# Kernel optimization log

Measured on AMD Instinct MI355X. Metric: run time of the kernel, lower is better.

The kernel has to match this reference:

```python
import jax, jax.numpy as jnp
import numpy as np

B, N, S = 8, 4096, 1024
D1, D2 = 128, 256
IN_CH, OUT_CH = D1 + D2, 256
BN_EPS = 1e-5


def setup_inputs() -> dict:
    key = jax.random.key(0)
    ks = jax.random.split(key, 12)
    inp = {
        "xyz1": jax.random.normal(ks[0], (B, N, 3), jnp.float32),
        "xyz2": jax.random.normal(ks[1], (B, S, 3), jnp.float32),
        "points1": jax.random.normal(ks[2], (B, N, D1), jnp.float32),
        "points2": jax.random.normal(ks[3], (B, S, D2), jnp.float32),
        # fuse: Conv1d(in_ch->out_ch, k=1) + BN
        "W_fuse": jax.random.normal(ks[4], (OUT_CH, IN_CH), jnp.float32) * (1.0 / np.sqrt(IN_CH)),
        "b_fuse": jnp.zeros((OUT_CH,), jnp.float32),
        "g_fuse": jnp.ones((OUT_CH,), jnp.float32),
        "bt_fuse": jnp.zeros((OUT_CH,), jnp.float32),
        # res block net1: Conv1d(out_ch->out_ch) + BN (res_expansion=1.0)
        "W1": jax.random.normal(ks[5], (OUT_CH, OUT_CH), jnp.float32) * (1.0 / np.sqrt(OUT_CH)),
        "b1": jnp.zeros((OUT_CH,), jnp.float32),
        "g1": jnp.ones((OUT_CH,), jnp.float32),
        "bt1": jnp.zeros((OUT_CH,), jnp.float32),
        # res block net2: Conv1d(out_ch->out_ch) + BN
        "W2": jax.random.normal(ks[6], (OUT_CH, OUT_CH), jnp.float32) * (1.0 / np.sqrt(OUT_CH)),
        "b2": jnp.zeros((OUT_CH,), jnp.float32),
        "g2": jnp.ones((OUT_CH,), jnp.float32),
        "bt2": jnp.zeros((OUT_CH,), jnp.float32),
    }
    return inp


def _bn(x, g, b):
    # BatchNorm1d training-mode forward: stats over (batch, length), x: [B, C, L]
    m = jnp.mean(x, axis=(0, 2), keepdims=True)
    v = jnp.var(x, axis=(0, 2), keepdims=True)
    return (x - m) * jax.lax.rsqrt(v + BN_EPS) * g[None, :, None] + b[None, :, None]


def _conv1x1(x, W, b):
    # x: [B, C_in, L], W: [C_out, C_in] -> [B, C_out, L]
    return jnp.einsum("oc,bcl->bol", W, x) + b[None, :, None]


def _gelu(x):
    return jax.nn.gelu(x, approximate=False)  # torch nn.GELU default (erf)


def reference(xyz1, xyz2, points1, points2,
              W_fuse, b_fuse, g_fuse, bt_fuse,
              W1, b1, g1, bt1, W2, b2, g2, bt2):
    # squared pairwise distances [B, N, S] without B x N x S x 3 intermediate
    d = (jnp.sum(xyz1 * xyz1, -1)[:, :, None]
         - 2.0 * jnp.einsum("bnc,bsc->bns", xyz1, xyz2)
         + jnp.sum(xyz2 * xyz2, -1)[:, None, :])
    # 3 nearest coarse points per dense point (== sort ascending, take first 3)
    neg_d3, idx = jax.lax.top_k(-d, 3)            # [B, N, 3]
    d3 = -neg_d3
    recip = 1.0 / (d3 + 1e-8)
    w = recip / jnp.sum(recip, axis=2, keepdims=True)  # [B, N, 3]
    gathered = points2[jnp.arange(points2.shape[0])[:, None, None], idx]  # [B, N, 3, D2]
    interp = jnp.sum(gathered * w[..., None], axis=2)  # [B, N, D2]

    new_points = jnp.concatenate([points1, interp], axis=-1)  # [B, N, D1+D2]
    x = jnp.transpose(new_points, (0, 2, 1))                   # [B, C, N]

    # fuse: conv-bn-gelu
    x = _gelu(_bn(_conv1x1(x, W_fuse, b_fuse), g_fuse, bt_fuse))
    # residual block: gelu(bn(conv(gelu(bn(conv(x))))) + x)
    y = _gelu(_bn(_conv1x1(x, W1, b1), g1, bt1))
    y = _bn(_conv1x1(y, W2, b2), g2, bt2)
    x = _gelu(y + x)

    return jnp.transpose(x, (0, 2, 1))  # [B, N, out_ch]
```

## Files before the change

kernel.cpp:

```cpp
#include <hip/hip_runtime.h>
#include <hip/hip_bf16.h>

constexpr int Bb = 8, Nn = 4096, Ss = 1024;
constexpr int D1 = 128, D2 = 256, KIN = 384, OC = 256;
constexpr int L = Bb * Nn;
constexpr float BN_EPS = 1e-5f;

typedef __attribute__((ext_vector_type(4))) float floatx4;
typedef __attribute__((ext_vector_type(8))) __bf16 bf16x8;

#define DEV __device__ __forceinline__

DEV float bf2f(unsigned short u) {
    union { unsigned int i; float f; } v; v.i = ((unsigned int)u) << 16; return v.f;
}
DEV unsigned short f2bf(float f) {
    union { float f; unsigned int i; } v; v.f = f;
    unsigned int x = v.i;
    return (unsigned short)((x + 0x7FFFu + ((x >> 16) & 1u)) >> 16);
}
DEV float gelu_f(float x) {
    float u = x * (0.7978845608f + 0.0356774081f * x * x);
    float t = __expf(-2.0f * u);
    return x * __builtin_amdgcn_rcpf(1.0f + t);
}

__global__ void k_probe(const unsigned int* __restrict__ w, int* __restrict__ flag) {
    if (threadIdx.x == 0 && blockIdx.x == 0) {
        int sane = 0;
        for (int i = 0; i < 64; ++i) {
            unsigned int lo = w[i] & 0xFFFFu;
            int e = (int)((lo >> 7) & 0xFF);
            if (e >= 100 && e <= 144) ++sane;
        }
        *flag = (sane >= 48) ? 0 : 1;
    }
}

__global__ void k_zero(float* p) {
    int i = blockIdx.x * 256 + threadIdx.x;
    if (i < 6 * 256) p[i] = 0.0f;
}

__global__ void k_prep_w(const void* __restrict__ src, unsigned short* __restrict__ dst,
                         int n, const int* __restrict__ dflag) {
    int i = blockIdx.x * 256 + threadIdx.x;
    if (i >= n) return;
    if (*dflag) dst[i] = f2bf(((const float*)src)[i]);
    else        dst[i] = ((const unsigned short*)src)[i];
}

DEV void merge3(float& d0, float& d1, float& d2, int& i0, int& i1, int& i2,
                float e0, float e1, float e2, int j0, int j1, int j2, bool pref) {
    float a0 = d0, a1 = d1, a2 = d2; int x0 = i0, x1 = i1, x2 = i2;
    float b0 = e0, b1 = e1;          int y0 = j0, y1 = j1;
    bool t = pref ? (a0 <= b0) : (a0 < b0);
    d0 = t ? a0 : b0; i0 = t ? x0 : y0;
    a0 = t ? a1 : a0; x0 = t ? x1 : x0;
    a1 = t ? a2 : a1; x1 = t ? x2 : x1;
    b0 = t ? b0 : b1; y0 = t ? y0 : y1;
    b1 = t ? b1 : e2; y1 = t ? y1 : j2;
    t = pref ? (a0 <= b0) : (a0 < b0);
    d1 = t ? a0 : b0; i1 = t ? x0 : y0;
    a0 = t ? a1 : a0; x0 = t ? x1 : x0;
    b0 = t ? b0 : b1; y0 = t ? y0 : y1;
    t = pref ? (a0 <= b0) : (a0 < b0);
    d2 = t ? a0 : b0; i2 = t ? x0 : y0;
}

__global__ __launch_bounds__(256) void k_nn(const void* __restrict__ xyz1_,
                                            const void* __restrict__ xyz2_,
                                            const int* __restrict__ dflag,
                                            int* __restrict__ nn_idx, float* __restrict__ nn_w) {
    __shared__ alignas(16) float s4[Ss * 4 + 32];
    int tid = threadIdx.x;
    int b = (blockIdx.x * 32) >> 12;
    bool isf = (*dflag != 0);

    if (isf) {
        const float* p2 = (const float*)xyz2_ + (size_t)b * Ss * 3;
        for (int i = tid; i < Ss * 3; i += 256) {
            int s = i / 3, k = i - s * 3;
            s4[s * 4 + k + ((s >> 7) << 2)] = p2[i];
        }
    } else {
        const unsigned short* p2 = (const unsigned short*)xyz2_ + (size_t)b * Ss * 3;
        for (int i = tid; i < Ss * 3; i += 256) {
            int s = i / 3, k = i - s * 3;
            s4[s * 4 + k + ((s >> 7) << 2)] = bf2f(p2[i]);
        }
    }
    __syncthreads();
    for (int s = tid; s < Ss; s += 256) {
        int a = s * 4 + ((s >> 7) << 2);
        float x = s4[a], y = s4[a + 1], z = s4[a + 2];
        s4[a + 3] = x * x + y * y + z * z;
    }
    __syncthreads();

    int part = tid & 7;
    int bn = blockIdx.x * 32 + (tid >> 3);
    float x1, y1, z1;
    if (isf) {
        const float* p1 = (const float*)xyz1_ + (size_t)bn * 3;
        x1 = p1[0]; y1 = p1[1]; z1 = p1[2];
    } else {
        const unsigned short* p1 = (const unsigned short*)xyz1_ + (size_t)bn * 3;
        x1 = bf2f(p1[0]); y1 = bf2f(p1[1]); z1 = bf2f(p1[2]);
    }
    float n1 = x1 * x1 + y1 * y1 + z1 * z1;

    float d0 = 3.4e38f, d1 = 3.4e38f, d2 = 3.4e38f;
    int i0 = 0, i1 = 0, i2 = 0;
    const float* sp = &s4[part * 516];
#pragma unroll 4
    for (int j = 0; j < 128; ++j) {
        float4 q = *(const float4*)(sp + j * 4);
        float d = n1 + q.w - 2.0f * (x1 * q.x + y1 * q.y + z1 * q.z);
        int s = part * 128 + j;
        bool c2 = d < d2, c1 = d < d1, c0 = d < d0;
        d2 = c1 ? d1 : (c2 ? d : d2); i2 = c1 ? i1 : (c2 ? s : i2);
        d1 = c0 ? d0 : (c1 ? d : d1); i1 = c0 ? i0 : (c1 ? s : i1);
        d0 = c0 ? d  : d0;            i0 = c0 ? s  : i0;
    }
#pragma unroll
    for (int m = 1; m <= 4; m <<= 1) {
        float e0 = __shfl_xor(d0, m, 64), e1 = __shfl_xor(d1, m, 64), e2 = __shfl_xor(d2, m, 64);
        int   j0 = __shfl_xor(i0, m, 64), j1 = __shfl_xor(i1, m, 64), j2 = __shfl_xor(i2, m, 64);
        bool pref = (part < (part ^ m));
        merge3(d0, d1, d2, i0, i1, i2, e0, e1, e2, j0, j1, j2, pref);
    }
    if (part == 0) {
        float r0 = 1.0f / (d0 + 1e-8f), r1 = 1.0f / (d1 + 1e-8f), r2 = 1.0f / (d2 + 1e-8f);
        float rs = 1.0f / (r0 + r1 + r2);
        nn_idx[bn * 3 + 0] = i0; nn_idx[bn * 3 + 1] = i1; nn_idx[bn * 3 + 2] = i2;
        nn_w[bn * 3 + 0] = r0 * rs; nn_w[bn * 3 + 1] = r1 * rs; nn_w[bn * 3 + 2] = r2 * rs;
    }
}

__global__ __launch_bounds__(256) void k_build_x(const void* __restrict__ points1_,
                                                 const void* __restrict__ points2_,
                                                 const int* __restrict__ dflag,
                                                 const int* __restrict__ nn_idx,
                                                 const float* __restrict__ nn_w,
                                                 unsigned short* __restrict__ X) {
    int tid = threadIdx.x;
    int pt = blockIdx.x * 4 + (tid >> 6);
    int lane = tid & 63;
    int b = pt >> 12;
    bool isf = (*dflag != 0);

    int i0 = nn_idx[pt * 3], i1 = nn_idx[pt * 3 + 1], i2 = nn_idx[pt * 3 + 2];
    float w0 = nn_w[pt * 3], w1 = nn_w[pt * 3 + 1], w2 = nn_w[pt * 3 + 2];
    int c = lane * 4;

    if (isf) {
        const float* p1 = (const float*)points1_ + (size_t)pt * D1;
        float2 v = *(const float2*)(p1 + lane * 2);
        unsigned int packed = (unsigned int)f2bf(v.x) | ((unsigned int)f2bf(v.y) << 16);
        ((unsigned int*)(X + (size_t)pt * KIN))[lane] = packed;

        const float* base = (const float*)points2_;
        const float* r0 = base + ((size_t)(b * Ss + i0)) * D2 + c;
        const float* r1 = base + ((size_t)(b * Ss + i1)) * D2 + c;
        const float* r2 = base + ((size_t)(b * Ss + i2)) * D2 + c;
        float4 a0 = *(const float4*)r0;
        float4 a1 = *(const float4*)r1;
        float4 a2 = *(const float4*)r2;
        uint2 out;
        unsigned short* uo = (unsigned short*)&out;
        uo[0] = f2bf(w0 * a0.x + w1 * a1.x + w2 * a2.x);
        uo[1] = f2bf(w0 * a0.y + w1 * a1.y + w2 * a2.y);
        uo[2] = f2bf(w0 * a0.z + w1 * a1.z + w2 * a2.z);
        uo[3] = f2bf(w0 * a0.w + w1 * a1.w + w2 * a2.w);
        *(uint2*)(X + (size_t)pt * KIN + D1 + c) = out;
    } else {
        const unsigned short* p1 = (const unsigned short*)points1_;
        ((unsigned int*)(X + (size_t)pt * KIN))[lane] =
            ((const unsigned int*)(p1 + (size_t)pt * D1))[lane];

        const unsigned short* base = (const unsigned short*)points2_;
        const unsigned short* r0 = base + ((size_t)(b * Ss + i0)) * D2 + c;
        const unsigned short* r1 = base + ((size_t)(b * Ss + i1)) * D2 + c;
        const unsigned short* r2 = base + ((size_t)(b * Ss + i2)) * D2 + c;
        uint2 v0 = *(const uint2*)r0;
        uint2 v1 = *(const uint2*)r1;
        uint2 v2 = *(const uint2*)r2;
        const unsigned short* u0 = (const unsigned short*)&v0;
        const unsigned short* u1 = (const unsigned short*)&v1;
        const unsigned short* u2 = (const unsigned short*)&v2;
        uint2 out;
        unsigned short* uo = (unsigned short*)&out;
#pragma unroll
        for (int j = 0; j < 4; ++j)
            uo[j] = f2bf(w0 * bf2f(u0[j]) + w1 * bf2f(u1[j]) + w2 * bf2f(u2[j]));
        *(uint2*)(X + (size_t)pt * KIN + D1 + c) = out;
    }
}

template <int K, int ACT>
__global__ __launch_bounds__(256) void k_gemm(const unsigned short* __restrict__ A,
                                              const unsigned short* __restrict__ W,
                                              unsigned short* __restrict__ Out,
                                              float* __restrict__ S1, float* __restrict__ S2,
                                              const float* __restrict__ cA,
                                              const float* __restrict__ cC) {
    __shared__ alignas(16) unsigned short As[128 * 64];
    __shared__ alignas(16) unsigned short Bs[128 * 64];
    __shared__ float sS1[128], sS2[128];

    int tid = threadIdx.x;
    int l0 = blockIdx.x * 128;
    int o0 = blockIdx.y * 128;
    int wave = tid >> 6, lane = tid & 63, quad = lane >> 4, lr = lane & 15;
    int wm = wave >> 1, wn = wave & 1;

    floatx4 zero4 = {0.f, 0.f, 0.f, 0.f};
    floatx4 acc[4][4];
#pragma unroll
    for (int mi = 0; mi < 4; ++mi)
#pragma unroll
        for (int ni = 0; ni < 4; ++ni) acc[mi][ni] = zero4;

    constexpr int KC = K / 64;
    for (int kc = 0; kc < KC; ++kc) {
        __syncthreads();
#pragma unroll
        for (int it = 0; it < 4; ++it) {
            int idx = it * 256 + tid;
            int row = idx >> 3, c8 = idx & 7;
            union { uint4 v; unsigned short u[8]; } va;
            va.v = *(const uint4*)(A + (size_t)(l0 + row) * K + kc * 64 + c8 * 8);
            if (ACT) {
                int kbase = kc * 64 + c8 * 8;
#pragma unroll
                for (int j = 0; j < 8; ++j) {
                    float f = bf2f(va.u[j]);
                    va.u[j] = f2bf(gelu_f(cA[kbase + j] * f + cC[kbase + j]));
                }
            }
            *(uint4*)&As[row * 64 + ((c8 ^ (row & 7)) << 3)] = va.v;

            uint4 vb = *(const uint4*)(W + (size_t)(o0 + row) * K + kc * 64 + c8 * 8);
            *(uint4*)&Bs[row * 64 + ((c8 ^ (row & 7)) << 3)] = vb;
        }
        __syncthreads();
#pragma unroll
        for (int ks8 = 0; ks8 < 2; ++ks8) {
            bf16x8 af[4], bfr[4];
#pragma unroll
            for (int mi = 0; mi < 4; ++mi) {
                int ra = wm * 64 + mi * 16 + lr;
                af[mi] = *(const bf16x8*)&As[ra * 64 + ((((ks8 << 2) + quad) ^ (ra & 7)) << 3)];
            }
#pragma unroll
            for (int ni = 0; ni < 4; ++ni) {
                int rb = wn * 64 + ni * 16 + lr;
                bfr[ni] = *(const bf16x8*)&Bs[rb * 64 + ((((ks8 << 2) + quad) ^ (rb & 7)) << 3)];
            }
#pragma unroll
            for (int mi = 0; mi < 4; ++mi)
#pragma unroll
                for (int ni = 0; ni < 4; ++ni)
                    acc[mi][ni] = __builtin_amdgcn_mfma_f32_16x16x32_bf16(af[mi], bfr[ni], acc[mi][ni], 0, 0, 0);
        }
    }

    float p1[4] = {0, 0, 0, 0}, p2[4] = {0, 0, 0, 0};
#pragma unroll
    for (int mi = 0; mi < 4; ++mi) {
#pragma unroll
        for (int ni = 0; ni < 4; ++ni) {
#pragma unroll
            for (int r = 0; r < 4; ++r) {
                float v = acc[mi][ni][r];
                int row = l0 + wm * 64 + mi * 16 + quad * 4 + r;
                int col = o0 + wn * 64 + ni * 16 + lr;
                Out[(size_t)row * OC + col] = f2bf(v);
                p1[ni] += v;
                p2[ni] += v * v;
            }
        }
    }
    if (tid < 128) { sS1[tid] = 0.f; sS2[tid] = 0.f; }
    __syncthreads();
#pragma unroll
    for (int ni = 0; ni < 4; ++ni) {
        atomicAdd(&sS1[wn * 64 + ni * 16 + lr], p1[ni]);
        atomicAdd(&sS2[wn * 64 + ni * 16 + lr], p2[ni]);
    }
    __syncthreads();
    if (tid < 128) {
        atomicAdd(&S1[o0 + tid], sS1[tid]);
        atomicAdd(&S2[o0 + tid], sS2[tid]);
    }
}

__global__ void k_finalize(const float* __restrict__ S1, const float* __restrict__ S2,
                           const void* __restrict__ g_, const void* __restrict__ bt_,
                           const int* __restrict__ dflag,
                           float* __restrict__ cA, float* __restrict__ cC) {
    int o = threadIdx.x;
    float m = S1[o] * (1.0f / (float)L);
    float var = S2[o] * (1.0f / (float)L) - m * m;
    float g, bt;
    if (*dflag) { g = ((const float*)g_)[o]; bt = ((const float*)bt_)[o]; }
    else { g = bf2f(((const unsigned short*)g_)[o]); bt = bf2f(((const unsigned short*)bt_)[o]); }
    float a = g * rsqrtf(var + BN_EPS);
    cA[o] = a;
    cC[o] = bt - m * a;
}

__global__ __launch_bounds__(256) void k_final(const unsigned short* __restrict__ t0,
                                               const unsigned short* __restrict__ t2,
                                               const float* __restrict__ cA0, const float* __restrict__ cC0,
                                               const float* __restrict__ cA2, const float* __restrict__ cC2,
                                               const int* __restrict__ dflag,
                                               void* __restrict__ out_) {
    int idx = (blockIdx.x * 256 + threadIdx.x) * 8;
    int col = idx & (OC - 1);
    union { uint4 v; unsigned short u[8]; } v0, v2;
    v0.v = *(const uint4*)(t0 + idx);
    v2.v = *(const uint4*)(t2 + idx);
    float r[8];
#pragma unroll
    for (int j = 0; j < 8; ++j) {
        float x = gelu_f(cA0[col + j] * bf2f(v0.u[j]) + cC0[col + j]);
        float y = cA2[col + j] * bf2f(v2.u[j]) + cC2[col + j];
        r[j] = gelu_f(x + y);
    }
    if (*dflag) {
        float* o = (float*)out_ + idx;
        float4 lo = {r[0], r[1], r[2], r[3]};
        float4 hi = {r[4], r[5], r[6], r[7]};
        *(float4*)o = lo;
        *(float4*)(o + 4) = hi;
    } else {
        union { uint4 v; unsigned short u[8]; } vo;
#pragma unroll
        for (int j = 0; j < 8; ++j) vo.u[j] = f2bf(r[j]);
        *(uint4*)((unsigned short*)out_ + idx) = vo.v;
    }
}

extern "C" void kernel_launch(void* const* d_in, const int* in_sizes, int n_in,
                              void* d_out, int out_size, void* d_ws, size_t ws_size,
                              hipStream_t stream) {
    const void* xyz1    = d_in[0];
    const void* xyz2    = d_in[1];
    const void* points1 = d_in[2];
    const void* points2 = d_in[3];
    const void* W_fuse  = d_in[4];
    const void* g_fuse  = d_in[6];
    const void* bt_fuse = d_in[7];
    const void* W1      = d_in[8];
    const void* g1      = d_in[10];
    const void* bt1     = d_in[11];
    const void* W2      = d_in[12];
    const void* g2      = d_in[14];
    const void* bt2     = d_in[15];

    char* ws = (char*)d_ws;
    unsigned short* X  = (unsigned short*)ws;
    unsigned short* t0 = (unsigned short*)(ws + 25165824);
    unsigned short* t1 = (unsigned short*)d_out;
    unsigned short* t2 = X;
    int*   nn_idx = (int*)(ws + 41943040);
    float* nn_w   = (float*)(ws + 42336256);
    float* stats  = (float*)(ws + 42729472);
    int*   dflag  = (int*)(ws + 42729472 + 3072 * 4);
    unsigned short* Wf_bf = (unsigned short*)(ws + 42745856);
    unsigned short* W1_bf = Wf_bf + 256 * KIN;
    unsigned short* W2_bf = W1_bf + 256 * OC;

    float *S1_0 = stats,        *S2_0 = stats + 256;
    float *S1_1 = stats + 512,  *S2_1 = stats + 768;
    float *S1_2 = stats + 1024, *S2_2 = stats + 1280;
    float *cA0 = stats + 1536, *cC0 = stats + 1792;
    float *cA1 = stats + 2048, *cC1 = stats + 2304;
    float *cA2 = stats + 2560, *cC2 = stats + 2816;

    k_probe<<<1, 64, 0, stream>>>((const unsigned int*)xyz1, dflag);
    k_zero<<<6, 256, 0, stream>>>(stats);
    k_prep_w<<<(256 * KIN + 255) / 256, 256, 0, stream>>>(W_fuse, Wf_bf, 256 * KIN, dflag);
    k_prep_w<<<(256 * OC + 255) / 256, 256, 0, stream>>>(W1, W1_bf, 256 * OC, dflag);
    k_prep_w<<<(256 * OC + 255) / 256, 256, 0, stream>>>(W2, W2_bf, 256 * OC, dflag);
    k_nn<<<L / 32, 256, 0, stream>>>(xyz1, xyz2, dflag, nn_idx, nn_w);
    k_build_x<<<L / 4, 256, 0, stream>>>(points1, points2, dflag, nn_idx, nn_w, X);

    dim3 ggrid(L / 128, 2);
    k_gemm<KIN, 0><<<ggrid, 256, 0, stream>>>(X, Wf_bf, t0, S1_0, S2_0, nullptr, nullptr);
    k_finalize<<<1, 256, 0, stream>>>(S1_0, S2_0, g_fuse, bt_fuse, dflag, cA0, cC0);
    k_gemm<OC, 1><<<ggrid, 256, 0, stream>>>(t0, W1_bf, t1, S1_1, S2_1, cA0, cC0);
    k_finalize<<<1, 256, 0, stream>>>(S1_1, S2_1, g1, bt1, dflag, cA1, cC1);
    k_gemm<OC, 1><<<ggrid, 256, 0, stream>>>(t1, W2_bf, t2, S1_2, S2_2, cA1, cC1);
    k_finalize<<<1, 256, 0, stream>>>(S1_2, S2_2, g2, bt2, dflag, cA2, cC2);
    k_final<<<L * OC / (256 * 8), 256, 0, stream>>>(t0, t2, cA0, cC0, cA2, cC2, dflag, d_out);
}
```

Baseline: 245.8 us.

## Retile GEMM to 64-row blocks covering all 256 outputs; merge setup kernels

The GEMM tile changes from 128x128, with two blocks per row tile, to 64 rows by all 256 output channels per block. The A tile, including its GELU/BN prologue in the ACT variants, is now loaded and activated once instead of twice. The cost is that each block reloads the full 256-row weight slice every K chunk, so weight traffic per output rises. The small setup kernels (probe+zero, three weight conversions) are also merged to cut launch count.

```diff
diff --git a/kernel.cpp b/kernel.cpp
--- a/kernel.cpp
+++ b/kernel.cpp
@@ -25,8 +25,10 @@
     return x * __builtin_amdgcn_rcpf(1.0f + t);
 }
 
-__global__ void k_probe(const unsigned int* __restrict__ w, int* __restrict__ flag) {
-    if (threadIdx.x == 0 && blockIdx.x == 0) {
+__global__ void k_init(float* stats, const unsigned int* __restrict__ w, int* __restrict__ flag) {
+    if (blockIdx.x < 6) {
+        stats[blockIdx.x * 256 + threadIdx.x] = 0.0f;
+    } else if (threadIdx.x == 0) {
         int sane = 0;
         for (int i = 0; i < 64; ++i) {
             unsigned int lo = w[i] & 0xFFFFu;
@@ -37,17 +39,16 @@
     }
 }
 
-__global__ void k_zero(float* p) {
+__global__ void k_prep_w(const void* __restrict__ s0, const void* __restrict__ s1,
+                         const void* __restrict__ s2, unsigned short* __restrict__ dst,
+                         const int* __restrict__ dflag) {
     int i = blockIdx.x * 256 + threadIdx.x;
-    if (i < 6 * 256) p[i] = 0.0f;
-}
-
-__global__ void k_prep_w(const void* __restrict__ src, unsigned short* __restrict__ dst,
-                         int n, const int* __restrict__ dflag) {
-    int i = blockIdx.x * 256 + threadIdx.x;
-    if (i >= n) return;
-    if (*dflag) dst[i] = f2bf(((const float*)src)[i]);
-    else        dst[i] = ((const unsigned short*)src)[i];
+    const void* src; int off;
+    if (i < 98304)      { src = s0; off = i; }
+    else if (i < 163840){ src = s1; off = i - 98304; }
+    else                { src = s2; off = i - 163840; }
+    if (*dflag) dst[i] = f2bf(((const float*)src)[off]);
+    else        dst[i] = ((const unsigned short*)src)[off];
 }
 
 DEV void merge3(float& d0, float& d1, float& d2, int& i0, int& i1, int& i2,
@@ -205,15 +206,13 @@
                                               float* __restrict__ S1, float* __restrict__ S2,
                                               const float* __restrict__ cA,
                                               const float* __restrict__ cC) {
-    __shared__ alignas(16) unsigned short As[128 * 64];
-    __shared__ alignas(16) unsigned short Bs[128 * 64];
-    __shared__ float sS1[128], sS2[128];
+    __shared__ alignas(16) unsigned short As[64 * 64];
+    __shared__ alignas(16) unsigned short Bs[256 * 64];
+    __shared__ float sS1[256], sS2[256];
 
     int tid = threadIdx.x;
-    int l0 = blockIdx.x * 128;
-    int o0 = blockIdx.y * 128;
-    int wave = tid >> 6, lane = tid & 63, quad = lane >> 4, lr = lane & 15;
-    int wm = wave >> 1, wn = wave & 1;
+    int l0 = blockIdx.x * 64;
+    int wn = tid >> 6, lane = tid & 63, quad = lane >> 4, lr = lane & 15;
 
     floatx4 zero4 = {0.f, 0.f, 0.f, 0.f};
     floatx4 acc[4][4];
@@ -226,7 +225,7 @@
     for (int kc = 0; kc < KC; ++kc) {
         __syncthreads();
 #pragma unroll
-        for (int it = 0; it < 4; ++it) {
+        for (int it = 0; it < 2; ++it) {
             int idx = it * 256 + tid;
             int row = idx >> 3, c8 = idx & 7;
             union { uint4 v; unsigned short u[8]; } va;
@@ -240,8 +239,12 @@
                 }
             }
             *(uint4*)&As[row * 64 + ((c8 ^ (row & 7)) << 3)] = va.v;
-
-            uint4 vb = *(const uint4*)(W + (size_t)(o0 + row) * K + kc * 64 + c8 * 8);
+        }
+#pragma unroll
+        for (int it = 0; it < 8; ++it) {
+            int idx = it * 256 + tid;
+            int row = idx >> 3, c8 = idx & 7;
+            uint4 vb = *(const uint4*)(W + (size_t)row * K + kc * 64 + c8 * 8);
             *(uint4*)&Bs[row * 64 + ((c8 ^ (row & 7)) << 3)] = vb;
         }
         __syncthreads();
@@ -250,7 +253,7 @@
             bf16x8 af[4], bfr[4];
 #pragma unroll
             for (int mi = 0; mi < 4; ++mi) {
-                int ra = wm * 64 + mi * 16 + lr;
+                int ra = mi * 16 + lr;
                 af[mi] = *(const bf16x8*)&As[ra * 64 + ((((ks8 << 2) + quad) ^ (ra & 7)) << 3)];
             }
 #pragma unroll
@@ -274,15 +277,15 @@
 #pragma unroll
             for (int r = 0; r < 4; ++r) {
                 float v = acc[mi][ni][r];
-                int row = l0 + wm * 64 + mi * 16 + quad * 4 + r;
-                int col = o0 + wn * 64 + ni * 16 + lr;
+                int row = l0 + mi * 16 + quad * 4 + r;
+                int col = wn * 64 + ni * 16 + lr;
                 Out[(size_t)row * OC + col] = f2bf(v);
                 p1[ni] += v;
                 p2[ni] += v * v;
             }
         }
     }
-    if (tid < 128) { sS1[tid] = 0.f; sS2[tid] = 0.f; }
+    sS1[tid] = 0.f; sS2[tid] = 0.f;
     __syncthreads();
 #pragma unroll
     for (int ni = 0; ni < 4; ++ni) {
@@ -290,10 +293,8 @@
         atomicAdd(&sS2[wn * 64 + ni * 16 + lr], p2[ni]);
     }
     __syncthreads();
-    if (tid < 128) {
-        atomicAdd(&S1[o0 + tid], sS1[tid]);
-        atomicAdd(&S2[o0 + tid], sS2[tid]);
-    }
+    atomicAdd(&S1[tid], sS1[tid]);
+    atomicAdd(&S2[tid], sS2[tid]);
 }
 
 __global__ void k_finalize(const float* __restrict__ S1, const float* __restrict__ S2,
@@ -370,8 +371,6 @@
     float* stats  = (float*)(ws + 42729472);
     int*   dflag  = (int*)(ws + 42729472 + 3072 * 4);
     unsigned short* Wf_bf = (unsigned short*)(ws + 42745856);
-    unsigned short* W1_bf = Wf_bf + 256 * KIN;
-    unsigned short* W2_bf = W1_bf + 256 * OC;
 
     float *S1_0 = stats,        *S2_0 = stats + 256;
     float *S1_1 = stats + 512,  *S2_1 = stats + 768;
@@ -380,20 +379,16 @@
     float *cA1 = stats + 2048, *cC1 = stats + 2304;
     float *cA2 = stats + 2560, *cC2 = stats + 2816;
 
-    k_probe<<<1, 64, 0, stream>>>((const unsigned int*)xyz1, dflag);
-    k_zero<<<6, 256, 0, stream>>>(stats);
-    k_prep_w<<<(256 * KIN + 255) / 256, 256, 0, stream>>>(W_fuse, Wf_bf, 256 * KIN, dflag);
-    k_prep_w<<<(256 * OC + 255) / 256, 256, 0, stream>>>(W1, W1_bf, 256 * OC, dflag);
-    k_prep_w<<<(256 * OC + 255) / 256, 256, 0, stream>>>(W2, W2_bf, 256 * OC, dflag);
+    k_init<<<7, 256, 0, stream>>>(stats, (const unsigned int*)xyz1, dflag);
+    k_prep_w<<<(98304 + 2 * 65536) / 256, 256, 0, stream>>>(W_fuse, W1, W2, Wf_bf, dflag);
     k_nn<<<L / 32, 256, 0, stream>>>(xyz1, xyz2, dflag, nn_idx, nn_w);
     k_build_x<<<L / 4, 256, 0, stream>>>(points1, points2, dflag, nn_idx, nn_w, X);
 
-    dim3 ggrid(L / 128, 2);
-    k_gemm<KIN, 0><<<ggrid, 256, 0, stream>>>(X, Wf_bf, t0, S1_0, S2_0, nullptr, nullptr);
+    k_gemm<KIN, 0><<<L / 64, 256, 0, stream>>>(X, Wf_bf, t0, S1_0, S2_0, nullptr, nullptr);
     k_finalize<<<1, 256, 0, stream>>>(S1_0, S2_0, g_fuse, bt_fuse, dflag, cA0, cC0);
-    k_gemm<OC, 1><<<ggrid, 256, 0, stream>>>(t0, W1_bf, t1, S1_1, S2_1, cA0, cC0);
+    k_gemm<OC, 1><<<L / 64, 256, 0, stream>>>(t0, Wf_bf + 98304, t1, S1_1, S2_1, cA0, cC0);
     k_finalize<<<1, 256, 0, stream>>>(S1_1, S2_1, g1, bt1, dflag, cA1, cC1);
-    k_gemm<OC, 1><<<ggrid, 256, 0, stream>>>(t1, W2_bf, t2, S1_2, S2_2, cA1, cC1);
+    k_gemm<OC, 1><<<L / 64, 256, 0, stream>>>(t1, Wf_bf + 163840, t2, S1_2, S2_2, cA1, cC1);
     k_finalize<<<1, 256, 0, stream>>>(S1_2, S2_2, g2, bt2, dflag, cA2, cC2);
     k_final<<<L * OC / (256 * 8), 256, 0, stream>>>(t0, t2, cA0, cC0, cA2, cC2, dflag, d_out);
 }
```

After: 247.8 us. Within noise of the previous version (+0.8%).
